# Kernel tuning notes

Measured on AMD Instinct MI355X. Metric: run time of the kernel, lower is better.

The kernel has to match this reference:

```python
import jax, jax.numpy as jnp
import numpy as np

B, T, K, C, H = 64, 20, 5, 3, 224  # batch, candidate frames, selected frames, channels, full res
LOWD = T * 3 * 64 * 64             # 245760 flattened low-res clip


def setup_inputs() -> dict:
    key = jax.random.key(0)
    ks = jax.random.split(key, 6)
    return {
        "Full_Frame64": jax.random.normal(ks[0], (B, T, 3, 64, 64), jnp.float32),
        "Full_Frame224": jax.random.normal(ks[1], (B, T, C, H, H), jnp.float32),
        "W_skim": jax.random.normal(ks[2], (LOWD, 64), jnp.float32) * 0.01,
        "b_skim": jnp.zeros((64,), jnp.float32),
        "W_pol": jax.random.normal(ks[3], (64, 20), jnp.float32) * 0.1,
        "b_pol": jnp.zeros((20,), jnp.float32),
        "W_eval": jax.random.normal(ks[4], (K * C, 400), jnp.float32) * 0.1,
        "b_eval": jnp.zeros((400,), jnp.float32),
    }


def reference(Full_Frame64, Full_Frame224, W_skim, b_skim, W_pol, b_pol, W_eval, b_eval):
    # skim_net stub: flatten low-res clip -> 64-d feature
    fea = Full_Frame64.reshape(B, -1) @ W_skim + b_skim                 # [B,64]
    # PolicyNet (per source bug, the inner Linear(64,64) is discarded): relu -> Linear(64,20)
    logits = jax.nn.relu(fea) @ W_pol + b_pol                           # [B,20]
    dist = jax.lax.stop_gradient(jax.nn.softmax(logits, axis=1))        # detached, as in source
    # Test mode: top-5 probabilities, indices sorted ascending
    idx = jnp.sort(jax.lax.top_k(dist, K)[1], axis=1)                   # [B,5] int32
    # gather selected frames: [B,5,3,224,224]
    selected = jnp.take_along_axis(Full_Frame224, idx[:, :, None, None, None], axis=1)
    # eval_net stub: spatial mean pool -> flatten -> Linear(15,400)
    pooled = selected.mean(axis=(3, 4)).reshape(B, K * C)               # [B,15]
    out = pooled @ W_eval + b_eval                                       # [B,400]
    return out
```

## Files before the change

### kernel.cpp

```cpp
#include <hip/hip_runtime.h>
#include <float.h>

#define B_SZ   64
#define T_FR   20
#define K_SEL  5
#define C_CH   3
#define D_SKIM 245760
#define HW224  50176
#define F4_IMG 12544
#define K1_BLOCKS 768
#define K1_TILES  10
#define BK        32
#define GP_PARTS  4
#define F4_PART   3136

#define AC(v, dp) ((dp) == 0 ? (v).x : (dp) == 1 ? (v).y : (dp) == 2 ? (v).z : (v).w)

__global__ __launch_bounds__(256) void skim_gemm(
    const float* __restrict__ A, const float* __restrict__ W,
    float* __restrict__ partial) {
  __shared__ float lds[12288];
  const int t    = threadIdx.x;
  const int lane = t & 63;
  const int wav  = t >> 6;
  const int kb   = lane >> 3;
  const int b0   = kb << 3;
  const int j0   = (lane & 7) << 3;

  const int ga0    = 2 * wav;
  const int arow0  = 8 * ga0 + (lane >> 3);
  const int aslot0 = (lane & 7) ^ (ga0 & 7);
  const int arow1  = 8 * (ga0 + 1) + (lane >> 3);
  const int aslot1 = (lane & 7) ^ ((ga0 + 1) & 7);
  const int wrow0  = 4 * ga0 + (lane >> 4);
  const int wcol0  = (lane & 15) << 2;
  const int wrow1  = 4 * (ga0 + 1) + (lane >> 4);

  float acc[8][8];
#pragma unroll
  for (int i = 0; i < 8; ++i)
#pragma unroll
    for (int j = 0; j < 8; ++j) acc[i][j] = 0.f;

  const long dbase = (long)blockIdx.x * (K1_TILES * BK);

#define STAGE(bufsel, tile_)                                                   \
  {                                                                            \
    const long d0_ = dbase + (long)(tile_) * BK;                               \
    float* Ab = lds + (bufsel) * 4096;                                         \
    float* Wb = Ab + 2048;                                                     \
    __builtin_amdgcn_global_load_lds(                                          \
        (const __attribute__((address_space(1))) void*)(A + (long)arow0 * D_SKIM + d0_ + aslot0 * 4), \
        (__attribute__((address_space(3))) void*)(Ab + ga0 * 256), 16, 0, 0);  \
    __builtin_amdgcn_global_load_lds(                                          \
        (const __attribute__((address_space(1))) void*)(A + (long)arow1 * D_SKIM + d0_ + aslot1 * 4), \
        (__attribute__((address_space(3))) void*)(Ab + (ga0 + 1) * 256), 16, 0, 0); \
    __builtin_amdgcn_global_load_lds(                                          \
        (const __attribute__((address_space(1))) void*)(W + (d0_ + wrow0) * 64 + wcol0), \
        (__attribute__((address_space(3))) void*)(Wb + ga0 * 256), 16, 0, 0);  \
    __builtin_amdgcn_global_load_lds(                                          \
        (const __attribute__((address_space(1))) void*)(W + (d0_ + wrow1) * 64 + wcol0), \
        (__attribute__((address_space(3))) void*)(Wb + (ga0 + 1) * 256), 16, 0, 0); \
  }

  STAGE(0, 0)
  STAGE(1, 1)

  for (int tile = 0; tile < K1_TILES; ++tile) {
    if (tile < K1_TILES - 1) {
      asm volatile("s_waitcnt vmcnt(4)" ::: "memory");
    } else {
      asm volatile("s_waitcnt vmcnt(0)" ::: "memory");
    }
    __builtin_amdgcn_sched_barrier(0);
    __builtin_amdgcn_s_barrier();
    __builtin_amdgcn_sched_barrier(0);
    if (tile + 2 < K1_TILES) STAGE((tile + 2) % 3, tile + 2)
    const float* Ab = lds + (tile % 3) * 4096;
    const float* Wb = Ab + 2048;
#pragma unroll
    for (int chunk = 0; chunk < 2; ++chunk) {
      const int dc = (wav << 3) + (chunk << 2);
      const int sw = dc ^ (kb << 2);
      const float4 a0 = *reinterpret_cast<const float4*>(&Ab[(b0 + 0) * 32 + sw]);
      const float4 a1 = *reinterpret_cast<const float4*>(&Ab[(b0 + 1) * 32 + sw]);
      const float4 a2 = *reinterpret_cast<const float4*>(&Ab[(b0 + 2) * 32 + sw]);
      const float4 a3 = *reinterpret_cast<const float4*>(&Ab[(b0 + 3) * 32 + sw]);
      const float4 a4 = *reinterpret_cast<const float4*>(&Ab[(b0 + 4) * 32 + sw]);
      const float4 a5 = *reinterpret_cast<const float4*>(&Ab[(b0 + 5) * 32 + sw]);
      const float4 a6 = *reinterpret_cast<const float4*>(&Ab[(b0 + 6) * 32 + sw]);
      const float4 a7 = *reinterpret_cast<const float4*>(&Ab[(b0 + 7) * 32 + sw]);
#pragma unroll
      for (int dp = 0; dp < 4; ++dp) {
        const float4 wlo = *reinterpret_cast<const float4*>(&Wb[(dc + dp) * 64 + j0]);
        const float4 whi = *reinterpret_cast<const float4*>(&Wb[(dc + dp) * 64 + j0 + 4]);
#define FMA_ROW(i, av)                             \
        acc[i][0] = fmaf(av, wlo.x, acc[i][0]);    \
        acc[i][1] = fmaf(av, wlo.y, acc[i][1]);    \
        acc[i][2] = fmaf(av, wlo.z, acc[i][2]);    \
        acc[i][3] = fmaf(av, wlo.w, acc[i][3]);    \
        acc[i][4] = fmaf(av, whi.x, acc[i][4]);    \
        acc[i][5] = fmaf(av, whi.y, acc[i][5]);    \
        acc[i][6] = fmaf(av, whi.z, acc[i][6]);    \
        acc[i][7] = fmaf(av, whi.w, acc[i][7]);
        FMA_ROW(0, AC(a0, dp)) FMA_ROW(1, AC(a1, dp))
        FMA_ROW(2, AC(a2, dp)) FMA_ROW(3, AC(a3, dp))
        FMA_ROW(4, AC(a4, dp)) FMA_ROW(5, AC(a5, dp))
        FMA_ROW(6, AC(a6, dp)) FMA_ROW(7, AC(a7, dp))
#undef FMA_ROW
      }
    }
  }
#undef STAGE

  __syncthreads();
  float* reg = lds + ((wav & 1) ? 4096 : 0);
  if (wav < 2) {
#pragma unroll
    for (int i = 0; i < 8; ++i) {
      *reinterpret_cast<float4*>(&reg[(b0 + i) * 64 + j0])     =
          make_float4(acc[i][0], acc[i][1], acc[i][2], acc[i][3]);
      *reinterpret_cast<float4*>(&reg[(b0 + i) * 64 + j0 + 4]) =
          make_float4(acc[i][4], acc[i][5], acc[i][6], acc[i][7]);
    }
  }
  __syncthreads();
  if (wav >= 2) {
#pragma unroll
    for (int i = 0; i < 8; ++i) {
      float4 lo = *reinterpret_cast<const float4*>(&reg[(b0 + i) * 64 + j0]);
      float4 hi = *reinterpret_cast<const float4*>(&reg[(b0 + i) * 64 + j0 + 4]);
      lo.x += acc[i][0]; lo.y += acc[i][1]; lo.z += acc[i][2]; lo.w += acc[i][3];
      hi.x += acc[i][4]; hi.y += acc[i][5]; hi.z += acc[i][6]; hi.w += acc[i][7];
      *reinterpret_cast<float4*>(&reg[(b0 + i) * 64 + j0])     = lo;
      *reinterpret_cast<float4*>(&reg[(b0 + i) * 64 + j0 + 4]) = hi;
    }
  }
  __syncthreads();
  const float4* r0 = reinterpret_cast<const float4*>(lds);
  const float4* r1 = reinterpret_cast<const float4*>(lds + 4096);
  float4* outp = reinterpret_cast<float4*>(partial + (long)blockIdx.x * 4096);
#pragma unroll
  for (int k = 0; k < 4; ++k) {
    const int e = t + k * 256;
    float4 v0 = r0[e], v1 = r1[e];
    outp[e] = make_float4(v0.x + v1.x, v0.y + v1.y, v0.z + v1.z, v0.w + v1.w);
  }
}

__global__ __launch_bounds__(256) void policy_topk(
    const float* __restrict__ partial, const float* __restrict__ b_skim,
    const float* __restrict__ W_pol, const float* __restrict__ b_pol,
    int* __restrict__ idx_out) {
  const int b    = blockIdx.x;
  const int t    = threadIdx.x;
  const int lane = t & 63;
  const int wav  = t >> 6;
  __shared__ float red[4][64];
  __shared__ float vsh[64];
  __shared__ float lgsh[20];

  const int P4 = K1_BLOCKS / 4;
  const float* base = partial + (long)(wav * P4) * 4096 + b * 64 + lane;
  float s = 0.f;
#pragma unroll 16
  for (int p = 0; p < P4; ++p) s += base[(long)p * 4096];
  red[wav][lane] = s;
  __syncthreads();

  if (wav == 0) {
    float fea = ((red[0][lane] + red[1][lane]) + (red[2][lane] + red[3][lane]))
                + b_skim[lane];
    vsh[lane] = fmaxf(fea, 0.f);
  }
  __syncthreads();

  if (t < 20) {
    float lg = b_pol[t];
#pragma unroll 8
    for (int k = 0; k < 64; ++k) lg = fmaf(vsh[k], W_pol[k * 20 + t], lg);
    lgsh[t] = lg;
  }
  __syncthreads();

  if (t == 0) {
    float lg[20];
#pragma unroll
    for (int i = 0; i < 20; ++i) lg[i] = lgsh[i];
    int sel[K_SEL];
#pragma unroll
    for (int s5 = 0; s5 < K_SEL; ++s5) {
      int bi = 0; float bv = lg[0];
      for (int i = 1; i < 20; ++i)
        if (lg[i] > bv) { bv = lg[i]; bi = i; }
      sel[s5] = bi; lg[bi] = -FLT_MAX;
    }
#pragma unroll
    for (int a = 1; a < K_SEL; ++a) {
      int v = sel[a], c = a;
      while (c > 0 && sel[c - 1] > v) { sel[c] = sel[c - 1]; --c; }
      sel[c] = v;
    }
#pragma unroll
    for (int s5 = 0; s5 < K_SEL; ++s5) idx_out[b * K_SEL + s5] = sel[s5];
  }
}

__global__ __launch_bounds__(256) void gather_pool(
    const float* __restrict__ F224, const int* __restrict__ idx,
    float* __restrict__ pooled_part) {
  const int blk  = blockIdx.x;
  const int part = blk & 3;
  const int img  = blk >> 2;
  const int b = img / 15;
  const int r = img % 15;
  const int s = r / 3;
  const int c = r % 3;
  const int fr = idx[b * K_SEL + s];
  const float4* p4 = reinterpret_cast<const float4*>(F224) +
      ((long)(b * T_FR + fr) * C_CH + c) * F4_IMG + part * F4_PART;
  float sum = 0.f;
#pragma unroll 4
  for (int i = threadIdx.x; i < F4_PART; i += 256) {
    float4 v = p4[i];
    sum += (v.x + v.y) + (v.z + v.w);
  }
#pragma unroll
  for (int off = 32; off; off >>= 1) sum += __shfl_down(sum, off);
  __shared__ float red[4];
  if ((threadIdx.x & 63) == 0) red[threadIdx.x >> 6] = sum;
  __syncthreads();
  if (threadIdx.x == 0) pooled_part[blk] = (red[0] + red[1]) + (red[2] + red[3]);
}

__global__ __launch_bounds__(512) void eval_gemm(
    const float* __restrict__ pooled_part, const float* __restrict__ W_eval,
    const float* __restrict__ b_eval, float* __restrict__ out) {
  const int b = blockIdx.x;
  const int t = threadIdx.x;
  __shared__ float sh[60];
  __shared__ float pk[15];
  if (t < 60) sh[t] = pooled_part[b * 60 + t];
  __syncthreads();
  if (t < 15)
    pk[t] = ((sh[t * 4] + sh[t * 4 + 1]) + (sh[t * 4 + 2] + sh[t * 4 + 3]))
            * (1.0f / HW224);
  __syncthreads();
  if (t < 400) {
    float o = b_eval[t];
#pragma unroll
    for (int k = 0; k < 15; ++k) o = fmaf(pk[k], W_eval[k * 400 + t], o);
    out[b * 400 + t] = o;
  }
}

extern "C" void kernel_launch(void* const* d_in, const int* in_sizes, int n_in,
                              void* d_out, int out_size, void* d_ws, size_t ws_size,
                              hipStream_t stream) {
  const float* F64    = (const float*)d_in[0];
  const float* F224   = (const float*)d_in[1];
  const float* W_skim = (const float*)d_in[2];
  const float* b_skim = (const float*)d_in[3];
  const float* W_pol  = (const float*)d_in[4];
  const float* b_pol  = (const float*)d_in[5];
  const float* W_eval = (const float*)d_in[6];
  const float* b_eval = (const float*)d_in[7];
  float* out = (float*)d_out;

  char* ws = (char*)d_ws;
  float* partial     = (float*)ws;
  int*   idx         = (int*)(ws + (size_t)K1_BLOCKS * 4096 * 4);
  float* pooled_part = (float*)(ws + (size_t)K1_BLOCKS * 4096 * 4 + 1280);

  skim_gemm  <<<K1_BLOCKS, 256, 0, stream>>>(F64, W_skim, partial);
  policy_topk<<<B_SZ, 256, 0, stream>>>(partial, b_skim, W_pol, b_pol, idx);
  gather_pool<<<B_SZ * K_SEL * C_CH * GP_PARTS, 256, 0, stream>>>(F224, idx, pooled_part);
  eval_gemm  <<<B_SZ, 512, 0, stream>>>(pooled_part, W_eval, b_eval, out);
}
```

Measured before the change: 88.48 us.

## Give each wave private LDS staging buffers and drop per-tile block barrier

Each wave now stages only its own 8-wide K slice of A and W into a private LDS region with its own triple buffer. This removes the block-wide s_barrier each tile, and the wave synchronises on its own vmcnt alone. The next tile's prefetch is issued after compute rather than before it, which may reduce how much load latency is overlapped. The swizzle and address math are also simplified to one row per lane.

```diff
diff --git a/kernel.cpp b/kernel.cpp
--- a/kernel.cpp
+++ b/kernel.cpp
@@ -14,7 +14,7 @@
 #define GP_PARTS  4
 #define F4_PART   3136
 
-#define AC(v, dp) ((dp) == 0 ? (v).x : (dp) == 1 ? (v).y : (dp) == 2 ? (v).z : (v).w)
+#define AC(v, kk) ((kk) == 0 ? (v).x : (kk) == 1 ? (v).y : (kk) == 2 ? (v).z : (v).w)
 
 __global__ __launch_bounds__(256) void skim_gemm(
     const float* __restrict__ A, const float* __restrict__ W,
@@ -25,16 +25,13 @@
   const int wav  = t >> 6;
   const int kb   = lane >> 3;
   const int b0   = kb << 3;
-  const int j0   = (lane & 7) << 3;
-
-  const int ga0    = 2 * wav;
-  const int arow0  = 8 * ga0 + (lane >> 3);
-  const int aslot0 = (lane & 7) ^ (ga0 & 7);
-  const int arow1  = 8 * (ga0 + 1) + (lane >> 3);
-  const int aslot1 = (lane & 7) ^ ((ga0 + 1) & 7);
-  const int wrow0  = 4 * ga0 + (lane >> 4);
-  const int wcol0  = (lane & 15) << 2;
-  const int wrow1  = 4 * (ga0 + 1) + (lane >> 4);
+  const int jo   = lane & 7;
+  const int j0   = jo << 3;
+
+  const int arow = lane ^ ((lane >> 3) & 7);
+  const int wrow = lane >> 4;
+  const int wcol = (lane & 15) << 2;
+  float* mybuf = lds + wav * 3072;
 
   float acc[8][8];
 #pragma unroll
@@ -46,21 +43,21 @@
 
 #define STAGE(bufsel, tile_)                                                   \
   {                                                                            \
-    const long d0_ = dbase + (long)(tile_) * BK;                               \
-    float* Ab = lds + (bufsel) * 4096;                                         \
-    float* Wb = Ab + 2048;                                                     \
-    __builtin_amdgcn_global_load_lds(                                          \
-        (const __attribute__((address_space(1))) void*)(A + (long)arow0 * D_SKIM + d0_ + aslot0 * 4), \
-        (__attribute__((address_space(3))) void*)(Ab + ga0 * 256), 16, 0, 0);  \
-    __builtin_amdgcn_global_load_lds(                                          \
-        (const __attribute__((address_space(1))) void*)(A + (long)arow1 * D_SKIM + d0_ + aslot1 * 4), \
-        (__attribute__((address_space(3))) void*)(Ab + (ga0 + 1) * 256), 16, 0, 0); \
-    __builtin_amdgcn_global_load_lds(                                          \
-        (const __attribute__((address_space(1))) void*)(W + (d0_ + wrow0) * 64 + wcol0), \
-        (__attribute__((address_space(3))) void*)(Wb + ga0 * 256), 16, 0, 0);  \
-    __builtin_amdgcn_global_load_lds(                                          \
-        (const __attribute__((address_space(1))) void*)(W + (d0_ + wrow1) * 64 + wcol0), \
-        (__attribute__((address_space(3))) void*)(Wb + (ga0 + 1) * 256), 16, 0, 0); \
+    const long d0_ = dbase + (long)(tile_) * BK + (wav << 3);                  \
+    float* Ab = mybuf + (bufsel) * 1024;                                       \
+    float* Wb = Ab + 512;                                                      \
+    __builtin_amdgcn_global_load_lds(                                          \
+        (const __attribute__((address_space(1))) void*)(A + (long)arow * D_SKIM + d0_), \
+        (__attribute__((address_space(3))) void*)(Ab), 16, 0, 0);              \
+    __builtin_amdgcn_global_load_lds(                                          \
+        (const __attribute__((address_space(1))) void*)(A + (long)arow * D_SKIM + d0_ + 4), \
+        (__attribute__((address_space(3))) void*)(Ab + 256), 16, 0, 0);        \
+    __builtin_amdgcn_global_load_lds(                                          \
+        (const __attribute__((address_space(1))) void*)(W + (d0_ + wrow) * 64 + wcol), \
+        (__attribute__((address_space(3))) void*)(Wb), 16, 0, 0);              \
+    __builtin_amdgcn_global_load_lds(                                          \
+        (const __attribute__((address_space(1))) void*)(W + (d0_ + 4 + wrow) * 64 + wcol), \
+        (__attribute__((address_space(3))) void*)(Wb + 256), 16, 0, 0);        \
   }
 
   STAGE(0, 0)
@@ -73,27 +70,18 @@
       asm volatile("s_waitcnt vmcnt(0)" ::: "memory");
     }
     __builtin_amdgcn_sched_barrier(0);
-    __builtin_amdgcn_s_barrier();
-    __builtin_amdgcn_sched_barrier(0);
-    if (tile + 2 < K1_TILES) STAGE((tile + 2) % 3, tile + 2)
-    const float* Ab = lds + (tile % 3) * 4096;
-    const float* Wb = Ab + 2048;
-#pragma unroll
-    for (int chunk = 0; chunk < 2; ++chunk) {
-      const int dc = (wav << 3) + (chunk << 2);
-      const int sw = dc ^ (kb << 2);
-      const float4 a0 = *reinterpret_cast<const float4*>(&Ab[(b0 + 0) * 32 + sw]);
-      const float4 a1 = *reinterpret_cast<const float4*>(&Ab[(b0 + 1) * 32 + sw]);
-      const float4 a2 = *reinterpret_cast<const float4*>(&Ab[(b0 + 2) * 32 + sw]);
-      const float4 a3 = *reinterpret_cast<const float4*>(&Ab[(b0 + 3) * 32 + sw]);
-      const float4 a4 = *reinterpret_cast<const float4*>(&Ab[(b0 + 4) * 32 + sw]);
-      const float4 a5 = *reinterpret_cast<const float4*>(&Ab[(b0 + 5) * 32 + sw]);
-      const float4 a6 = *reinterpret_cast<const float4*>(&Ab[(b0 + 6) * 32 + sw]);
-      const float4 a7 = *reinterpret_cast<const float4*>(&Ab[(b0 + 7) * 32 + sw]);
+    const float* Ab = mybuf + (tile % 3) * 1024;
+    const float* Wb = Ab + 512;
+#pragma unroll
+    for (int c = 0; c < 2; ++c) {
+      float4 a[8];
+#pragma unroll
+      for (int i = 0; i < 8; ++i)
+        a[i] = *reinterpret_cast<const float4*>(&Ab[c * 256 + (((b0 + i) ^ kb) << 2)]);
 #pragma unroll
       for (int dp = 0; dp < 4; ++dp) {
-        const float4 wlo = *reinterpret_cast<const float4*>(&Wb[(dc + dp) * 64 + j0]);
-        const float4 whi = *reinterpret_cast<const float4*>(&Wb[(dc + dp) * 64 + j0 + 4]);
+        const float4 wlo = *reinterpret_cast<const float4*>(&Wb[(c * 4 + dp) * 64 + j0]);
+        const float4 whi = *reinterpret_cast<const float4*>(&Wb[(c * 4 + dp) * 64 + j0 + 4]);
 #define FMA_ROW(i, av)                             \
         acc[i][0] = fmaf(av, wlo.x, acc[i][0]);    \
         acc[i][1] = fmaf(av, wlo.y, acc[i][1]);    \
@@ -103,13 +91,15 @@
         acc[i][5] = fmaf(av, whi.y, acc[i][5]);    \
         acc[i][6] = fmaf(av, whi.z, acc[i][6]);    \
         acc[i][7] = fmaf(av, whi.w, acc[i][7]);
-        FMA_ROW(0, AC(a0, dp)) FMA_ROW(1, AC(a1, dp))
-        FMA_ROW(2, AC(a2, dp)) FMA_ROW(3, AC(a3, dp))
-        FMA_ROW(4, AC(a4, dp)) FMA_ROW(5, AC(a5, dp))
-        FMA_ROW(6, AC(a6, dp)) FMA_ROW(7, AC(a7, dp))
+        FMA_ROW(0, AC(a[0], dp)) FMA_ROW(1, AC(a[1], dp))
+        FMA_ROW(2, AC(a[2], dp)) FMA_ROW(3, AC(a[3], dp))
+        FMA_ROW(4, AC(a[4], dp)) FMA_ROW(5, AC(a[5], dp))
+        FMA_ROW(6, AC(a[6], dp)) FMA_ROW(7, AC(a[7], dp))
 #undef FMA_ROW
       }
     }
+    __builtin_amdgcn_sched_barrier(0);
+    if (tile + 2 < K1_TILES) STAGE((tile + 2) % 3, tile + 2)
   }
 #undef STAGE
 
```

Result: faster. 85.99 us (-2.8%).
